# Optimization experiments

Measured on AMD Instinct MI355X. Metric: run time of the kernel, lower is better.

## Reference

```python
import jax, jax.numpy as jnp
import numpy as np

B, SQ, SK, D, H, DFF = 4, 1024, 1024, 1024, 16, 4096
DEPTH = D // H
EPS = 1e-6


def setup_inputs() -> dict:
    key = jax.random.key(0)
    ks = jax.random.split(key, 32)
    s = 0.02
    inp = {
        "x": jax.random.normal(ks[0], (B, SQ, D), jnp.float32),
        "y": jax.random.normal(ks[1], (B, SK, D), jnp.float32),
        "causality_mask": jnp.zeros((1, 1, 1, SK), jnp.float32),
        "padding_mask": jnp.zeros((1, 1, SQ, SQ), jnp.float32),
    }
    names = ["sa_wq", "sa_wk", "sa_wv", "sa_wo", "ca_wq", "ca_wk", "ca_wv", "ca_wo"]
    for i, n in enumerate(names):
        inp[n] = jax.random.normal(ks[2 + i], (D, D), jnp.float32) * s
        inp[n.replace("w", "b")] = jnp.zeros((D,), jnp.float32)
    inp["ffn_w1"] = jax.random.normal(ks[10], (D, DFF), jnp.float32) * s
    inp["ffn_b1"] = jnp.zeros((DFF,), jnp.float32)
    inp["ffn_w2"] = jax.random.normal(ks[11], (DFF, D), jnp.float32) * s
    inp["ffn_b2"] = jnp.zeros((D,), jnp.float32)
    for i, n in enumerate(["ln1", "ln2", "ln3"]):
        inp[n + "_g"] = jnp.ones((D,), jnp.float32)
        inp[n + "_b"] = jnp.zeros((D,), jnp.float32)
    return inp


def _layernorm(x, g, b):
    mu = jnp.mean(x, axis=-1, keepdims=True)
    var = jnp.mean(jnp.square(x - mu), axis=-1, keepdims=True)
    return (x - mu) * jax.lax.rsqrt(var + EPS) * g + b


def _split_heads(x):
    b, s, _ = x.shape
    return x.reshape(b, s, H, DEPTH).transpose(0, 2, 1, 3)  # [B,H,S,depth]


def _mha(q_in, k_in, v_in, mask, wq, bq, wk, bk, wv, bv, wo, bo):
    q = _split_heads(q_in @ wq + bq)
    k = _split_heads(k_in @ wk + bk)
    v = _split_heads(v_in @ wv + bv)
    scores = jnp.einsum("bhqd,bhkd->bhqk", q, k) / jnp.sqrt(jnp.float32(DEPTH))
    if mask is not None:
        scores = scores + mask * -1e9
    attn = jax.nn.softmax(scores, axis=-1)
    out = jnp.einsum("bhqk,bhkd->bhqd", attn, v)
    out = out.transpose(0, 2, 1, 3).reshape(q_in.shape[0], q_in.shape[1], D)
    return out @ wo + bo, attn


def reference(x, y, causality_mask, padding_mask,
              sa_wq, sa_bq, sa_wk, sa_bk, sa_wv, sa_bv, sa_wo, sa_bo,
              ca_wq, ca_bq, ca_wk, ca_bk, ca_wv, ca_bv, ca_wo, ca_bo,
              ffn_w1, ffn_b1, ffn_w2, ffn_b2,
              ln1_g, ln1_b, ln2_g, ln2_b, ln3_g, ln3_b):
    # self-attn sub-layer (source passes padding_mask here)
    residual = x
    out = _layernorm(x, ln1_g, ln1_b)
    out, dec_attn = _mha(out, out, out, padding_mask,
                         sa_wq, sa_bq, sa_wk, sa_bk, sa_wv, sa_bv, sa_wo, sa_bo)
    out = out + residual
    # cross-attn sub-layer (source passes causality_mask here)
    residual = out
    out2 = _layernorm(out, ln2_g, ln2_b)
    out2, dec_enc_attn = _mha(out2, y, y, causality_mask,
                              ca_wq, ca_bq, ca_wk, ca_bk, ca_wv, ca_bv, ca_wo, ca_bo)
    out = out2 + residual
    # FFN sub-layer
    residual = out
    h = _layernorm(out, ln3_g, ln3_b)
    h = jax.nn.relu(h @ ffn_w1 + ffn_b1) @ ffn_w2 + ffn_b2
    out = h + residual
    return out, dec_attn, dec_enc_attn
```

## Files before the change

### kernel.cpp

```cpp
#include <hip/hip_runtime.h>
#include <stdint.h>


typedef __attribute__((ext_vector_type(8))) short bf16x8;
typedef __attribute__((ext_vector_type(4))) float f32x4;

typedef const void __attribute__((address_space(1)))* gas_ptr;
typedef void __attribute__((address_space(3)))* las_ptr;

__device__ __forceinline__ ushort f2bf(float f) {
  union { float f; uint32_t u; } x; x.f = f;
  uint32_t r = x.u + 0x7fffu + ((x.u >> 16) & 1u);
  return (ushort)(r >> 16);
}


__global__ __launch_bounds__(256) void convert_f32_bf16(const float* __restrict__ src,
                                                        ushort* __restrict__ dst, int n4) {
  int i = blockIdx.x * 256 + threadIdx.x;
  if (i < n4) {
    float4 v = ((const float4*)src)[i];
    ushort4 o;
    o.x = f2bf(v.x); o.y = f2bf(v.y); o.z = f2bf(v.z); o.w = f2bf(v.w);
    ((ushort4*)dst)[i] = o;
  }
}

__global__ __launch_bounds__(256) void transpose_f32_bf16(const float* __restrict__ src,
                                                          ushort* __restrict__ dst,
                                                          int R, int C) {
  __shared__ ushort tile[32][33];
  int c0 = blockIdx.x * 32, r0 = blockIdx.y * 32;
  int tx = threadIdx.x, ty = threadIdx.y;
  for (int i = ty; i < 32; i += 8)
    tile[i][tx] = f2bf(src[(long)(r0 + i) * C + c0 + tx]);
  __syncthreads();
  for (int i = ty; i < 32; i += 8)
    dst[(long)(c0 + i) * R + r0 + tx] = tile[tx][i];
}

__global__ __launch_bounds__(256) void layernorm_to_bf16(const float* __restrict__ x,
                                                         const float* __restrict__ gamma,
                                                         const float* __restrict__ beta,
                                                         ushort* __restrict__ out) {
  const int row = blockIdx.x;
  const int t = threadIdx.x, lane = t & 63, w = t >> 6;
  float4 v = ((const float4*)(x + (long)row * 1024))[t];
  float s = v.x + v.y + v.z + v.w;
#pragma unroll
  for (int off = 32; off >= 1; off >>= 1) s += __shfl_xor(s, off);
  __shared__ float r1[4], r2[4];
  if (lane == 0) r1[w] = s;
  __syncthreads();
  const float mu = (r1[0] + r1[1] + r1[2] + r1[3]) * (1.f / 1024.f);
  const float dx = v.x - mu, dy = v.y - mu, dz = v.z - mu, dw = v.w - mu;
  float q = dx * dx + dy * dy + dz * dz + dw * dw;
#pragma unroll
  for (int off = 32; off >= 1; off >>= 1) q += __shfl_xor(q, off);
  if (lane == 0) r2[w] = q;
  __syncthreads();
  const float var = (r2[0] + r2[1] + r2[2] + r2[3]) * (1.f / 1024.f);
  const float is = rsqrtf(var + 1e-6f);
  float4 g4 = ((const float4*)gamma)[t];
  float4 b4 = ((const float4*)beta)[t];
  ushort4 o;
  o.x = f2bf(dx * is * g4.x + b4.x);
  o.y = f2bf(dy * is * g4.y + b4.y);
  o.z = f2bf(dz * is * g4.z + b4.z);
  o.w = f2bf(dw * is * g4.w + b4.w);
  ((ushort4*)(out + (long)row * 1024))[t] = o;
}

__global__ __launch_bounds__(256) void init_bias_res(const float* __restrict__ res,
                                                     const float* __restrict__ bias,
                                                     float* __restrict__ out, int n4) {
  int i = blockIdx.x * 256 + threadIdx.x;
  if (i < n4) {
    float4 r = ((const float4*)res)[i];
    float4 b = ((const float4*)bias)[i & 255];
    float4 o = {r.x + b.x, r.y + b.y, r.z + b.z, r.w + b.w};
    ((float4*)out)[i] = o;
  }
}


constexpr int EPI_BF16 = 0;
constexpr int EPI_F32RES = 1;
constexpr int EPI_BF16RELU = 4;
constexpr int EPI_ATOMIC = 6;

template <int BM, int BN, int EPI>
__global__ __launch_bounds__(256) void gemm_bt(const ushort* __restrict__ Aall, long sAz, int lda,
                                               const ushort* __restrict__ Ball, long sBz, int ldb,
                                               const float* __restrict__ bias,
                                               const float* __restrict__ res,
                                               void* __restrict__ outv,
                                               int M, int N, int K) {
  constexpr int BK = 32;
  constexpr int WM = BM / 2, WN = BN / 2;
  constexpr int MR = WM / 16, NR = WN / 16;
  constexpr int ACH = BM * BK / 8;
  constexpr int BCH = BN * BK / 8;

  const int z = blockIdx.z;
  const ushort* A = Aall + (long)z * sAz;
  const ushort* B = Ball + (long)z * sBz;
  const int m0 = blockIdx.x * BM;
  const int n0 = blockIdx.y * BN;

  __shared__ ushort lds[2][(BM + BN) * BK];

  const int t = threadIdx.x;
  const int lane = t & 63;
  const int w = t >> 6;
  const int wr = w >> 1, wc = w & 1;
  const int g = lane >> 4, rl = lane & 15;
  const int cbase = t & ~63;

  f32x4 acc[MR][NR];
#pragma unroll
  for (int i = 0; i < MR; ++i)
#pragma unroll
    for (int j = 0; j < NR; ++j) {
      f32x4 zv = {0.f, 0.f, 0.f, 0.f};
      acc[i][j] = zv;
    }

  auto stage = [&](int buf, int kt) {
    const int k0 = kt * BK;
#pragma unroll
    for (int j = 0; j < ACH / 256; ++j) {
      const int c = j * 256 + t;
      const int row = c >> 2, pos = c & 3;
      const int kg = pos ^ (row & 3);
      const ushort* src = A + (long)(m0 + row) * lda + k0 + kg * 8;
      ushort* dst = &lds[buf][(j * 256 + cbase) * 8];
      __builtin_amdgcn_global_load_lds((gas_ptr)src, (las_ptr)dst, 16, 0, 0);
    }
#pragma unroll
    for (int j = 0; j < BCH / 256; ++j) {
      const int c = j * 256 + t;
      const int row = c >> 2, pos = c & 3;
      const int kg = pos ^ (row & 3);
      const ushort* src = B + (long)(n0 + row) * ldb + k0 + kg * 8;
      ushort* dst = &lds[buf][BM * BK + (j * 256 + cbase) * 8];
      __builtin_amdgcn_global_load_lds((gas_ptr)src, (las_ptr)dst, 16, 0, 0);
    }
  };

  const int nt = K / BK;
  stage(0, 0);
  asm volatile("s_waitcnt vmcnt(0)" ::: "memory");
  __syncthreads();

  int cur = 0;
  for (int kt = 0; kt < nt; ++kt) {
    if (kt + 1 < nt) stage(cur ^ 1, kt + 1);
    bf16x8 af[MR], bfr[NR];
#pragma unroll
    for (int i = 0; i < MR; ++i) {
      const int row = wr * WM + i * 16 + rl;
      af[i] = *(const bf16x8*)&lds[cur][row * BK + ((g ^ (row & 3)) * 8)];
    }
#pragma unroll
    for (int j = 0; j < NR; ++j) {
      const int row = wc * WN + j * 16 + rl;
      bfr[j] = *(const bf16x8*)&lds[cur][BM * BK + row * BK + ((g ^ (row & 3)) * 8)];
    }
#pragma unroll
    for (int i = 0; i < MR; ++i)
#pragma unroll
      for (int j = 0; j < NR; ++j)
        acc[i][j] = __builtin_amdgcn_mfma_f32_16x16x32_bf16(af[i], bfr[j], acc[i][j], 0, 0, 0);
    asm volatile("s_waitcnt vmcnt(0)" ::: "memory");
    __syncthreads();
    cur ^= 1;
  }

  const bool hasb = (bias != nullptr);
#pragma unroll
  for (int i = 0; i < MR; ++i) {
#pragma unroll
    for (int j = 0; j < NR; ++j) {
#pragma unroll
      for (int e = 0; e < 4; ++e) {
        const int row = m0 + wr * WM + i * 16 + g * 4 + e;
        const int col = n0 + wc * WN + j * 16 + rl;
        float v = acc[i][j][e];
        if (hasb) v += bias[col];
        if constexpr (EPI == EPI_BF16 || EPI == EPI_BF16RELU) {
          float vv = (EPI == EPI_BF16RELU && v < 0.f) ? 0.f : v;
          ((ushort*)outv)[(long)row * N + col] = f2bf(vv);
        } else if constexpr (EPI == EPI_F32RES) {
          ((float*)outv)[(long)row * N + col] = v + res[(long)row * N + col];
        } else if constexpr (EPI == EPI_ATOMIC) {
          atomicAdd(&((float*)outv)[(long)row * N + col], v);
        }
      }
    }
  }
}


template <bool CROSS>
__global__ __launch_bounds__(256) void qkv_proj(const ushort* __restrict__ Aq,
                                                const ushort* __restrict__ Akv,
                                                const ushort* __restrict__ Wt,
                                                const float* __restrict__ bq,
                                                const float* __restrict__ bk,
                                                const float* __restrict__ bv,
                                                ushort* __restrict__ Qh,
                                                ushort* __restrict__ Kh,
                                                ushort* __restrict__ VhT) {
  constexpr int BM = 128, BN = 128, BK = 32;
  constexpr int MR = 4, NR = 4;

  const int z = blockIdx.z;
  const ushort* A = (CROSS && z > 0) ? Akv : Aq;
  const ushort* B = Wt + (long)z * 1048576;
  const float* bias = (z == 0) ? bq : (z == 1) ? bk : bv;
  const int m0 = blockIdx.x * BM;
  const int n0 = blockIdx.y * BN;

  __shared__ ushort lds[2][(BM + BN) * BK];

  const int t = threadIdx.x;
  const int lane = t & 63;
  const int w = t >> 6;
  const int wr = w >> 1, wc = w & 1;
  const int g = lane >> 4, rl = lane & 15;
  const int cbase = t & ~63;

  f32x4 acc[MR][NR];
#pragma unroll
  for (int i = 0; i < MR; ++i)
#pragma unroll
    for (int j = 0; j < NR; ++j) {
      f32x4 zv = {0.f, 0.f, 0.f, 0.f};
      acc[i][j] = zv;
    }

  auto stage = [&](int buf, int kt) {
    const int k0 = kt * BK;
    {
      const int row = t >> 2, pos = t & 3;
      const int kg = pos ^ (row & 3);
      const ushort* srcA = A + (long)(m0 + row) * 1024 + k0 + kg * 8;
      __builtin_amdgcn_global_load_lds((gas_ptr)srcA, (las_ptr)&lds[buf][cbase * 8], 16, 0, 0);
      const int c2 = 256 + t;
      const int row2 = c2 >> 2, pos2 = c2 & 3;
      const int kg2 = pos2 ^ (row2 & 3);
      const ushort* srcA2 = A + (long)(m0 + row2) * 1024 + k0 + kg2 * 8;
      __builtin_amdgcn_global_load_lds((gas_ptr)srcA2, (las_ptr)&lds[buf][(256 + cbase) * 8], 16, 0, 0);
      const ushort* srcB = B + (long)(n0 + row) * 1024 + k0 + kg * 8;
      __builtin_amdgcn_global_load_lds((gas_ptr)srcB, (las_ptr)&lds[buf][4096 + cbase * 8], 16, 0, 0);
      const ushort* srcB2 = B + (long)(n0 + row2) * 1024 + k0 + kg2 * 8;
      __builtin_amdgcn_global_load_lds((gas_ptr)srcB2, (las_ptr)&lds[buf][4096 + (256 + cbase) * 8], 16, 0, 0);
    }
  };

  stage(0, 0);
  asm volatile("s_waitcnt vmcnt(0)" ::: "memory");
  __syncthreads();

  int cur = 0;
  for (int kt = 0; kt < 32; ++kt) {
    if (kt + 1 < 32) stage(cur ^ 1, kt + 1);
    bf16x8 af[MR], bfr[NR];
#pragma unroll
    for (int i = 0; i < MR; ++i) {
      const int row = wr * 64 + i * 16 + rl;
      af[i] = *(const bf16x8*)&lds[cur][row * BK + ((g ^ (row & 3)) * 8)];
    }
#pragma unroll
    for (int j = 0; j < NR; ++j) {
      const int row = wc * 64 + j * 16 + rl;
      bfr[j] = *(const bf16x8*)&lds[cur][4096 + row * BK + ((g ^ (row & 3)) * 8)];
    }
#pragma unroll
    for (int i = 0; i < MR; ++i)
#pragma unroll
      for (int j = 0; j < NR; ++j)
        acc[i][j] = __builtin_amdgcn_mfma_f32_16x16x32_bf16(af[i], bfr[j], acc[i][j], 0, 0, 0);
    asm volatile("s_waitcnt vmcnt(0)" ::: "memory");
    __syncthreads();
    cur ^= 1;
  }

  ushort* out = (z == 0) ? Qh : (z == 1) ? Kh : VhT;
#pragma unroll
  for (int i = 0; i < MR; ++i) {
#pragma unroll
    for (int j = 0; j < NR; ++j) {
#pragma unroll
      for (int e = 0; e < 4; ++e) {
        const int row = m0 + wr * 64 + i * 16 + g * 4 + e;
        const int col = n0 + wc * 64 + j * 16 + rl;
        const float v = acc[i][j][e] + bias[col];
        const int b = row >> 10, s = row & 1023, h = col >> 6, d = col & 63;
        if (z < 2)
          out[(((long)(b * 16 + h) * 1024) + s) * 64 + d] = f2bf(v);
        else
          out[((long)(b * 16 + h) * 64 + d) * 1024 + s] = f2bf(v);
      }
    }
  }
}


__device__ __forceinline__ int p_off(int r, int p) {
  return (r * 128 + (p ^ (r & 7))) * 8;
}

template <int MODE>
__global__ __launch_bounds__(512) void attn_softmax_pv(const ushort* __restrict__ Q,
                                                       const ushort* __restrict__ Kh,
                                                       const ushort* __restrict__ VhT,
                                                       const float* __restrict__ mask,
                                                       float* __restrict__ outF,
                                                       ushort* __restrict__ ctx) {
  const int bh = blockIdx.y;
  const int q0 = blockIdx.x * 32;
  const int t = threadIdx.x, lane = t & 63, w = t >> 6;
  const int g = lane >> 4, rl = lane & 15;
  const ushort* Qb = Q + (long)bh * 65536;
  const ushort* Kb = Kh + (long)bh * 65536;
  const ushort* Vb = VhT + (long)bh * 65536;

  __shared__ ushort Pl[32768];
  __shared__ float redm[8][32];
  __shared__ float reds[8][32];

  bf16x8 qa[2][2];
#pragma unroll
  for (int rb = 0; rb < 2; ++rb)
#pragma unroll
    for (int kk = 0; kk < 2; ++kk)
      qa[rb][kk] = *(const bf16x8*)(Qb + (long)(q0 + rb * 16 + rl) * 64 + kk * 32 + g * 8);

  f32x4 acc[2][8];
#pragma unroll
  for (int rb = 0; rb < 2; ++rb)
#pragma unroll
    for (int nf = 0; nf < 8; ++nf) {
      f32x4 zv = {0.f, 0.f, 0.f, 0.f};
      acc[rb][nf] = zv;
    }

  const int c0 = w * 128;
#pragma unroll
  for (int nf = 0; nf < 8; ++nf) {
    const ushort* kp = Kb + (long)(c0 + nf * 16 + rl) * 64 + g * 8;
    bf16x8 k0 = *(const bf16x8*)(kp);
    bf16x8 k1 = *(const bf16x8*)(kp + 32);
#pragma unroll
    for (int rb = 0; rb < 2; ++rb) {
      acc[rb][nf] = __builtin_amdgcn_mfma_f32_16x16x32_bf16(qa[rb][0], k0, acc[rb][nf], 0, 0, 0);
      acc[rb][nf] = __builtin_amdgcn_mfma_f32_16x16x32_bf16(qa[rb][1], k1, acc[rb][nf], 0, 0, 0);
    }
  }

#pragma unroll
  for (int rb = 0; rb < 2; ++rb)
#pragma unroll
    for (int nf = 0; nf < 8; ++nf)
#pragma unroll
      for (int e = 0; e < 4; ++e) {
        const int r = q0 + rb * 16 + g * 4 + e;
        const int c = c0 + nf * 16 + rl;
        float mv;
        if constexpr (MODE == 0) mv = mask[(long)r * 1024 + c];
        else mv = mask[c];
        acc[rb][nf][e] = acc[rb][nf][e] * 0.125f + mv * (-1e9f);
      }

  float mrow[2][4];
#pragma unroll
  for (int rb = 0; rb < 2; ++rb)
#pragma unroll
    for (int e = 0; e < 4; ++e) {
      float m = acc[rb][0][e];
#pragma unroll
      for (int nf = 1; nf < 8; ++nf) m = fmaxf(m, acc[rb][nf][e]);
#pragma unroll
      for (int off = 8; off >= 1; off >>= 1) m = fmaxf(m, __shfl_xor(m, off));
      mrow[rb][e] = m;
    }
  if (rl == 0)
#pragma unroll
    for (int rb = 0; rb < 2; ++rb)
#pragma unroll
      for (int e = 0; e < 4; ++e) redm[w][rb * 16 + g * 4 + e] = mrow[rb][e];
  __syncthreads();
  float mfin[2][4];
#pragma unroll
  for (int rb = 0; rb < 2; ++rb)
#pragma unroll
    for (int e = 0; e < 4; ++e) {
      const int r = rb * 16 + g * 4 + e;
      float m = redm[0][r];
#pragma unroll
      for (int ww = 1; ww < 8; ++ww) m = fmaxf(m, redm[ww][r]);
      mfin[rb][e] = m;
    }

  float srow[2][4];
#pragma unroll
  for (int rb = 0; rb < 2; ++rb)
#pragma unroll
    for (int e = 0; e < 4; ++e) {
      float s = 0.f;
#pragma unroll
      for (int nf = 0; nf < 8; ++nf) {
        float p = exp2f((acc[rb][nf][e] - mfin[rb][e]) * 1.44269504088896340736f);
        acc[rb][nf][e] = p;
        s += p;
      }
#pragma unroll
      for (int off = 8; off >= 1; off >>= 1) s += __shfl_xor(s, off);
      srow[rb][e] = s;
    }
  if (rl == 0)
#pragma unroll
    for (int rb = 0; rb < 2; ++rb)
#pragma unroll
      for (int e = 0; e < 4; ++e) reds[w][rb * 16 + g * 4 + e] = srow[rb][e];
  __syncthreads();

#pragma unroll
  for (int rb = 0; rb < 2; ++rb)
#pragma unroll
    for (int e = 0; e < 4; ++e) {
      const int r = rb * 16 + g * 4 + e;
      float s = 0.f;
#pragma unroll
      for (int ww = 0; ww < 8; ++ww) s += reds[ww][r];
      const float inv = 1.0f / s;
      const long rowoff = (long)bh * 1048576 + (long)(q0 + r) * 1024;
#pragma unroll
      for (int nf = 0; nf < 8; ++nf) {
        const int c = c0 + nf * 16 + rl;
        const float p = acc[rb][nf][e] * inv;
        outF[rowoff + c] = p;
        Pl[p_off(r, c >> 3) + (c & 7)] = f2bf(p);
      }
    }
  __syncthreads();

  f32x4 acc2[2][4];
#pragma unroll
  for (int rb = 0; rb < 2; ++rb)
#pragma unroll
    for (int j = 0; j < 4; ++j) {
      f32x4 zv = {0.f, 0.f, 0.f, 0.f};
      acc2[rb][j] = zv;
    }
#pragma unroll
  for (int s = 0; s < 4; ++s) {
    const int kb = c0 + s * 32;
    bf16x8 a[2];
#pragma unroll
    for (int rb = 0; rb < 2; ++rb)
      a[rb] = *(const bf16x8*)&Pl[p_off(rb * 16 + rl, (kb >> 3) + g)];
#pragma unroll
    for (int j = 0; j < 4; ++j) {
      bf16x8 b = *(const bf16x8*)(Vb + (long)(j * 16 + rl) * 1024 + kb + g * 8);
#pragma unroll
      for (int rb = 0; rb < 2; ++rb)
        acc2[rb][j] = __builtin_amdgcn_mfma_f32_16x16x32_bf16(a[rb], b, acc2[rb][j], 0, 0, 0);
    }
  }
  __syncthreads();

  float* Pred = (float*)Pl;
#pragma unroll
  for (int rb = 0; rb < 2; ++rb)
#pragma unroll
    for (int j = 0; j < 4; ++j)
#pragma unroll
      for (int e = 0; e < 4; ++e) {
        const int r = rb * 16 + g * 4 + e;
        const int d = j * 16 + rl;
        Pred[w * 2048 + r * 64 + d] = acc2[rb][j][e];
      }
  __syncthreads();

  const int bb = bh >> 4, hh = bh & 15;
#pragma unroll
  for (int i = t; i < 2048; i += 512) {
    float s = 0.f;
#pragma unroll
    for (int ww = 0; ww < 8; ++ww) s += Pred[ww * 2048 + i];
    const int r = i >> 6, d = i & 63;
    ctx[((long)bb * 1024 + q0 + r) * 1024 + hh * 64 + d] = f2bf(s);
  }
}


extern "C" void kernel_launch(void* const* d_in, const int* in_sizes, int n_in,
                              void* d_out, int out_size, void* d_ws, size_t ws_size,
                              hipStream_t stream) {
  (void)in_sizes; (void)n_in; (void)out_size; (void)ws_size;

  const float* x     = (const float*)d_in[0];
  const float* y     = (const float*)d_in[1];
  const float* cmask = (const float*)d_in[2];
  const float* pmask = (const float*)d_in[3];
  const float* sa_wq = (const float*)d_in[4];
  const float* sa_bq = (const float*)d_in[5];
  const float* sa_wk = (const float*)d_in[6];
  const float* sa_bk = (const float*)d_in[7];
  const float* sa_wv = (const float*)d_in[8];
  const float* sa_bv = (const float*)d_in[9];
  const float* sa_wo = (const float*)d_in[10];
  const float* sa_bo = (const float*)d_in[11];
  const float* ca_wq = (const float*)d_in[12];
  const float* ca_bq = (const float*)d_in[13];
  const float* ca_wk = (const float*)d_in[14];
  const float* ca_bk = (const float*)d_in[15];
  const float* ca_wv = (const float*)d_in[16];
  const float* ca_bv = (const float*)d_in[17];
  const float* ca_wo = (const float*)d_in[18];
  const float* ca_bo = (const float*)d_in[19];
  const float* ffn_w1 = (const float*)d_in[20];
  const float* ffn_b1 = (const float*)d_in[21];
  const float* ffn_w2 = (const float*)d_in[22];
  const float* ffn_b2 = (const float*)d_in[23];
  const float* ln1_g = (const float*)d_in[24];
  const float* ln1_b = (const float*)d_in[25];
  const float* ln2_g = (const float*)d_in[26];
  const float* ln2_b = (const float*)d_in[27];
  const float* ln3_g = (const float*)d_in[28];
  const float* ln3_b = (const float*)d_in[29];

  char* ws = (char*)d_ws;
  ushort* wT0 = (ushort*)(ws + 0);
  ushort* w1T = (ushort*)(ws + (16L << 20));
  ushort* w2T = (ushort*)(ws + (24L << 20));
  ushort* ybf = (ushort*)(ws + (32L << 20));
  ushort* lnb = (ushort*)(ws + (40L << 20));
  ushort* Qh  = (ushort*)(ws + (48L << 20));
  ushort* Kh  = (ushort*)(ws + (56L << 20));
  ushort* VhT = (ushort*)(ws + (64L << 20));
  ushort* ctx = (ushort*)(ws + (72L << 20));
  float*  out1 = (float*)(ws + (80L << 20));
  float*  out2 = (float*)(ws + (96L << 20));
  ushort* hbuf = (ushort*)(ws + (112L << 20));

  float* out0   = (float*)d_out;
  float* attnF1 = out0 + 4194304;
  float* attnF2 = out0 + 71303168;

  convert_f32_bf16<<<dim3(4096), dim3(256), 0, stream>>>(y, ybf, 1048576);
  const float* wsrc[8] = {sa_wq, sa_wk, sa_wv, sa_wo, ca_wq, ca_wk, ca_wv, ca_wo};
  for (int i = 0; i < 8; ++i)
    transpose_f32_bf16<<<dim3(32, 32), dim3(32, 8), 0, stream>>>(wsrc[i], wT0 + (long)i * 1048576, 1024, 1024);
  transpose_f32_bf16<<<dim3(128, 32), dim3(32, 8), 0, stream>>>(ffn_w1, w1T, 1024, 4096);
  transpose_f32_bf16<<<dim3(32, 128), dim3(32, 8), 0, stream>>>(ffn_w2, w2T, 4096, 1024);

  layernorm_to_bf16<<<dim3(4096), dim3(256), 0, stream>>>(x, ln1_g, ln1_b, lnb);

  qkv_proj<false><<<dim3(32, 8, 3), dim3(256), 0, stream>>>(
      lnb, lnb, wT0, sa_bq, sa_bk, sa_bv, Qh, Kh, VhT);

  attn_softmax_pv<0><<<dim3(32, 64), dim3(512), 0, stream>>>(Qh, Kh, VhT, pmask, attnF1, ctx);

  init_bias_res<<<dim3(4096), dim3(256), 0, stream>>>(x, sa_bo, out1, 1048576);
  gemm_bt<128, 128, EPI_ATOMIC><<<dim3(32, 8, 2), dim3(256), 0, stream>>>(
      ctx, 512L, 1024, wT0 + 3L * 1048576, 512L, 1024, nullptr, nullptr, out1, 4096, 1024, 512);

  layernorm_to_bf16<<<dim3(4096), dim3(256), 0, stream>>>(out1, ln2_g, ln2_b, lnb);

  qkv_proj<true><<<dim3(32, 8, 3), dim3(256), 0, stream>>>(
      lnb, ybf, wT0 + 4L * 1048576, ca_bq, ca_bk, ca_bv, Qh, Kh, VhT);

  attn_softmax_pv<1><<<dim3(32, 64), dim3(512), 0, stream>>>(Qh, Kh, VhT, cmask, attnF2, ctx);

  init_bias_res<<<dim3(4096), dim3(256), 0, stream>>>(out1, ca_bo, out2, 1048576);
  gemm_bt<128, 128, EPI_ATOMIC><<<dim3(32, 8, 2), dim3(256), 0, stream>>>(
      ctx, 512L, 1024, wT0 + 7L * 1048576, 512L, 1024, nullptr, nullptr, out2, 4096, 1024, 512);

  layernorm_to_bf16<<<dim3(4096), dim3(256), 0, stream>>>(out2, ln3_g, ln3_b, lnb);

  gemm_bt<128, 128, EPI_BF16RELU><<<dim3(32, 32, 1), dim3(256), 0, stream>>>(
      lnb, 0L, 1024, w1T, 0L, 1024, ffn_b1, nullptr, hbuf, 4096, 4096, 1024);

  init_bias_res<<<dim3(4096), dim3(256), 0, stream>>>(out2, ffn_b2, out0, 1048576);
  gemm_bt<128, 128, EPI_ATOMIC><<<dim3(32, 8, 4), dim3(256), 0, stream>>>(
      hbuf, 1024L, 4096, w2T, 1024L, 4096, nullptr, nullptr, out0, 4096, 1024, 1024);
}
```

Baseline: 1.212 ms.

## Deepen GEMM pipeline, replace atomics with partial-sum reduce+LN, add XCD tile mapping

The GEMM and QKV projection kernels now use a 4-buffer LDS ring with three stages in flight and vmcnt-based waits, instead of double buffering with a full drain every step. Split-K output GEMMs write per-split partials instead of doing float atomics. A new fused reduce_ln kernel sums the partials, adds bias and residual, and applies the next LayerNorm, which removes the init_bias_res and separate layernorm launches. Blocks are remapped so neighbouring tiles land on the same XCD for L2 reuse, the 8 weight transposes are batched into one launch, and the V-transpose epilogue stores packed ushort4. The partial buffers cost extra memory traffic and workspace, and the hard-coded vmcnt constants depend on the static_assert that each stage issues 4 loads.

```diff
diff --git a/kernel.cpp b/kernel.cpp
--- a/kernel.cpp
+++ b/kernel.cpp
@@ -24,6 +24,21 @@
     o.x = f2bf(v.x); o.y = f2bf(v.y); o.z = f2bf(v.z); o.w = f2bf(v.w);
     ((ushort4*)dst)[i] = o;
   }
+}
+
+struct Ptr8 { const float* p[8]; };
+
+__global__ __launch_bounds__(256) void transpose8_f32_bf16(Ptr8 srcs, ushort* __restrict__ dst) {
+  __shared__ ushort tile[32][33];
+  const float* src = srcs.p[blockIdx.z];
+  ushort* d = dst + (long)blockIdx.z * 1048576;
+  int c0 = blockIdx.x * 32, r0 = blockIdx.y * 32;
+  int tx = threadIdx.x, ty = threadIdx.y;
+  for (int i = ty; i < 32; i += 8)
+    tile[i][tx] = f2bf(src[(long)(r0 + i) * 1024 + c0 + tx]);
+  __syncthreads();
+  for (int i = ty; i < 32; i += 8)
+    d[(long)(c0 + i) * 1024 + r0 + tx] = tile[tx][i];
 }
 
 __global__ __launch_bounds__(256) void transpose_f32_bf16(const float* __restrict__ src,
@@ -71,29 +86,71 @@
   ((ushort4*)(out + (long)row * 1024))[t] = o;
 }
 
-__global__ __launch_bounds__(256) void init_bias_res(const float* __restrict__ res,
-                                                     const float* __restrict__ bias,
-                                                     float* __restrict__ out, int n4) {
-  int i = blockIdx.x * 256 + threadIdx.x;
-  if (i < n4) {
-    float4 r = ((const float4*)res)[i];
-    float4 b = ((const float4*)bias)[i & 255];
-    float4 o = {r.x + b.x, r.y + b.y, r.z + b.z, r.w + b.w};
-    ((float4*)out)[i] = o;
-  }
-}
-
-
-constexpr int EPI_BF16 = 0;
-constexpr int EPI_F32RES = 1;
-constexpr int EPI_BF16RELU = 4;
-constexpr int EPI_ATOMIC = 6;
-
-template <int BM, int BN, int EPI>
+template <int NP, bool DO_LN>
+__global__ __launch_bounds__(256) void reduce_ln(const float* __restrict__ part,
+                                                 const float* __restrict__ res,
+                                                 const float* __restrict__ bias,
+                                                 const float* __restrict__ g,
+                                                 const float* __restrict__ b,
+                                                 float* __restrict__ outres,
+                                                 ushort* __restrict__ outln) {
+  const int row = blockIdx.x;
+  const int t = threadIdx.x, lane = t & 63, w = t >> 6;
+  const long base = (long)row * 256 + t;
+  float4 v = ((const float4*)res)[base];
+  float4 bi = ((const float4*)bias)[t];
+  v.x += bi.x; v.y += bi.y; v.z += bi.z; v.w += bi.w;
+#pragma unroll
+  for (int p = 0; p < NP; ++p) {
+    float4 pv = ((const float4*)part)[(long)p * 1048576 + base];
+    v.x += pv.x; v.y += pv.y; v.z += pv.z; v.w += pv.w;
+  }
+  ((float4*)outres)[base] = v;
+  if constexpr (DO_LN) {
+    float s = v.x + v.y + v.z + v.w;
+#pragma unroll
+    for (int off = 32; off >= 1; off >>= 1) s += __shfl_xor(s, off);
+    __shared__ float r1[4], r2[4];
+    if (lane == 0) r1[w] = s;
+    __syncthreads();
+    const float mu = (r1[0] + r1[1] + r1[2] + r1[3]) * (1.f / 1024.f);
+    const float dx = v.x - mu, dy = v.y - mu, dz = v.z - mu, dw = v.w - mu;
+    float q = dx * dx + dy * dy + dz * dz + dw * dw;
+#pragma unroll
+    for (int off = 32; off >= 1; off >>= 1) q += __shfl_xor(q, off);
+    if (lane == 0) r2[w] = q;
+    __syncthreads();
+    const float var = (r2[0] + r2[1] + r2[2] + r2[3]) * (1.f / 1024.f);
+    const float is = rsqrtf(var + 1e-6f);
+    float4 g4 = ((const float4*)g)[t];
+    float4 b4 = ((const float4*)b)[t];
+    ushort4 o;
+    o.x = f2bf(dx * is * g4.x + b4.x);
+    o.y = f2bf(dy * is * g4.y + b4.y);
+    o.z = f2bf(dz * is * g4.z + b4.z);
+    o.w = f2bf(dw * is * g4.w + b4.w);
+    ((ushort4*)outln)[base] = o;
+  }
+}
+
+template <int MS, int NS>
+__device__ __forceinline__ void xcd_map(int& mi, int& ni) {
+  const int GX = gridDim.x;
+  const int bid = blockIdx.x + GX * blockIdx.y;
+  const int xcd = bid & 7, idx = bid >> 3;
+  const int mw = GX / MS;
+  mi = (xcd % MS) * mw + idx % mw;
+  ni = (xcd / MS) * (gridDim.y / NS) + idx / mw;
+}
+
+
+constexpr int EPI_BF16RELU = 0;
+constexpr int EPI_PARTIAL = 1;
+
+template <int BM, int BN, int EPI, int MS, int NS>
 __global__ __launch_bounds__(256) void gemm_bt(const ushort* __restrict__ Aall, long sAz, int lda,
                                                const ushort* __restrict__ Ball, long sBz, int ldb,
                                                const float* __restrict__ bias,
-                                               const float* __restrict__ res,
                                                void* __restrict__ outv,
                                                int M, int N, int K) {
   constexpr int BK = 32;
@@ -101,14 +158,18 @@
   constexpr int MR = WM / 16, NR = WN / 16;
   constexpr int ACH = BM * BK / 8;
   constexpr int BCH = BN * BK / 8;
+  constexpr int BUFSZ = (BM + BN) * BK;
+  static_assert((ACH + BCH) / 256 == 4, "LPT must be 4 for vmcnt constants");
 
   const int z = blockIdx.z;
   const ushort* A = Aall + (long)z * sAz;
   const ushort* B = Ball + (long)z * sBz;
-  const int m0 = blockIdx.x * BM;
-  const int n0 = blockIdx.y * BN;
-
-  __shared__ ushort lds[2][(BM + BN) * BK];
+  int mi, ni;
+  xcd_map<MS, NS>(mi, ni);
+  const int m0 = mi * BM;
+  const int n0 = ni * BN;
+
+  __shared__ ushort lds[4 * BUFSZ];
 
   const int t = threadIdx.x;
   const int lane = t & 63;
@@ -128,56 +189,60 @@
 
   auto stage = [&](int buf, int kt) {
     const int k0 = kt * BK;
-#pragma unroll
-    for (int j = 0; j < ACH / 256; ++j) {
+    ushort* lb = &lds[buf * BUFSZ];
+#pragma unroll
+    for (int j = 0; j < 2; ++j) {
       const int c = j * 256 + t;
       const int row = c >> 2, pos = c & 3;
       const int kg = pos ^ (row & 3);
       const ushort* src = A + (long)(m0 + row) * lda + k0 + kg * 8;
-      ushort* dst = &lds[buf][(j * 256 + cbase) * 8];
-      __builtin_amdgcn_global_load_lds((gas_ptr)src, (las_ptr)dst, 16, 0, 0);
-    }
-#pragma unroll
-    for (int j = 0; j < BCH / 256; ++j) {
+      __builtin_amdgcn_global_load_lds((gas_ptr)src, (las_ptr)&lb[(j * 256 + cbase) * 8], 16, 0, 0);
+    }
+#pragma unroll
+    for (int j = 0; j < 2; ++j) {
       const int c = j * 256 + t;
       const int row = c >> 2, pos = c & 3;
       const int kg = pos ^ (row & 3);
       const ushort* src = B + (long)(n0 + row) * ldb + k0 + kg * 8;
-      ushort* dst = &lds[buf][BM * BK + (j * 256 + cbase) * 8];
-      __builtin_amdgcn_global_load_lds((gas_ptr)src, (las_ptr)dst, 16, 0, 0);
+      __builtin_amdgcn_global_load_lds((gas_ptr)src, (las_ptr)&lb[BM * BK + (j * 256 + cbase) * 8], 16, 0, 0);
     }
   };
 
   const int nt = K / BK;
   stage(0, 0);
-  asm volatile("s_waitcnt vmcnt(0)" ::: "memory");
-  __syncthreads();
-
-  int cur = 0;
+  if (nt > 1) stage(1, 1);
+  if (nt > 2) stage(2, 2);
+
   for (int kt = 0; kt < nt; ++kt) {
-    if (kt + 1 < nt) stage(cur ^ 1, kt + 1);
+    const int rem = nt - 1 - kt;
+    if (rem >= 2)      asm volatile("s_waitcnt vmcnt(8)" ::: "memory");
+    else if (rem == 1) asm volatile("s_waitcnt vmcnt(4)" ::: "memory");
+    else               asm volatile("s_waitcnt vmcnt(0)" ::: "memory");
+    __builtin_amdgcn_s_barrier();
+    asm volatile("" ::: "memory");
+    const ushort* buf = &lds[(kt & 3) * BUFSZ];
     bf16x8 af[MR], bfr[NR];
 #pragma unroll
     for (int i = 0; i < MR; ++i) {
       const int row = wr * WM + i * 16 + rl;
-      af[i] = *(const bf16x8*)&lds[cur][row * BK + ((g ^ (row & 3)) * 8)];
+      af[i] = *(const bf16x8*)&buf[row * BK + ((g ^ (row & 3)) * 8)];
     }
 #pragma unroll
     for (int j = 0; j < NR; ++j) {
       const int row = wc * WN + j * 16 + rl;
-      bfr[j] = *(const bf16x8*)&lds[cur][BM * BK + row * BK + ((g ^ (row & 3)) * 8)];
+      bfr[j] = *(const bf16x8*)&buf[BM * BK + row * BK + ((g ^ (row & 3)) * 8)];
     }
 #pragma unroll
     for (int i = 0; i < MR; ++i)
 #pragma unroll
       for (int j = 0; j < NR; ++j)
         acc[i][j] = __builtin_amdgcn_mfma_f32_16x16x32_bf16(af[i], bfr[j], acc[i][j], 0, 0, 0);
-    asm volatile("s_waitcnt vmcnt(0)" ::: "memory");
-    __syncthreads();
-    cur ^= 1;
-  }
-
-  const bool hasb = (bias != nullptr);
+    asm volatile("s_waitcnt lgkmcnt(0)" ::: "memory");
+    __builtin_amdgcn_s_barrier();
+    asm volatile("" ::: "memory");
+    if (kt + 3 < nt) stage((kt + 3) & 3, kt + 3);
+  }
+
 #pragma unroll
   for (int i = 0; i < MR; ++i) {
 #pragma unroll
@@ -187,14 +252,11 @@
         const int row = m0 + wr * WM + i * 16 + g * 4 + e;
         const int col = n0 + wc * WN + j * 16 + rl;
         float v = acc[i][j][e];
-        if (hasb) v += bias[col];
-        if constexpr (EPI == EPI_BF16 || EPI == EPI_BF16RELU) {
-          float vv = (EPI == EPI_BF16RELU && v < 0.f) ? 0.f : v;
-          ((ushort*)outv)[(long)row * N + col] = f2bf(vv);
-        } else if constexpr (EPI == EPI_F32RES) {
-          ((float*)outv)[(long)row * N + col] = v + res[(long)row * N + col];
-        } else if constexpr (EPI == EPI_ATOMIC) {
-          atomicAdd(&((float*)outv)[(long)row * N + col], v);
+        if constexpr (EPI == EPI_BF16RELU) {
+          v += bias[col];
+          ((ushort*)outv)[(long)row * N + col] = f2bf(v < 0.f ? 0.f : v);
+        } else {
+          ((float*)outv)[(long)z * M * N + (long)row * N + col] = v;
         }
       }
     }
@@ -214,15 +276,18 @@
                                                 ushort* __restrict__ VhT) {
   constexpr int BM = 128, BN = 128, BK = 32;
   constexpr int MR = 4, NR = 4;
+  constexpr int BUFSZ = (BM + BN) * BK;
 
   const int z = blockIdx.z;
   const ushort* A = (CROSS && z > 0) ? Akv : Aq;
   const ushort* B = Wt + (long)z * 1048576;
   const float* bias = (z == 0) ? bq : (z == 1) ? bk : bv;
-  const int m0 = blockIdx.x * BM;
-  const int n0 = blockIdx.y * BN;
-
-  __shared__ ushort lds[2][(BM + BN) * BK];
+  int mi, ni;
+  xcd_map<4, 2>(mi, ni);
+  const int m0 = mi * BM;
+  const int n0 = ni * BN;
+
+  __shared__ ushort lds[4 * BUFSZ];
 
   const int t = threadIdx.x;
   const int lane = t & 63;
@@ -242,49 +307,57 @@
 
   auto stage = [&](int buf, int kt) {
     const int k0 = kt * BK;
-    {
-      const int row = t >> 2, pos = t & 3;
+    ushort* lb = &lds[buf * BUFSZ];
+#pragma unroll
+    for (int j = 0; j < 2; ++j) {
+      const int c = j * 256 + t;
+      const int row = c >> 2, pos = c & 3;
       const int kg = pos ^ (row & 3);
-      const ushort* srcA = A + (long)(m0 + row) * 1024 + k0 + kg * 8;
-      __builtin_amdgcn_global_load_lds((gas_ptr)srcA, (las_ptr)&lds[buf][cbase * 8], 16, 0, 0);
-      const int c2 = 256 + t;
-      const int row2 = c2 >> 2, pos2 = c2 & 3;
-      const int kg2 = pos2 ^ (row2 & 3);
-      const ushort* srcA2 = A + (long)(m0 + row2) * 1024 + k0 + kg2 * 8;
-      __builtin_amdgcn_global_load_lds((gas_ptr)srcA2, (las_ptr)&lds[buf][(256 + cbase) * 8], 16, 0, 0);
-      const ushort* srcB = B + (long)(n0 + row) * 1024 + k0 + kg * 8;
-      __builtin_amdgcn_global_load_lds((gas_ptr)srcB, (las_ptr)&lds[buf][4096 + cbase * 8], 16, 0, 0);
-      const ushort* srcB2 = B + (long)(n0 + row2) * 1024 + k0 + kg2 * 8;
-      __builtin_amdgcn_global_load_lds((gas_ptr)srcB2, (las_ptr)&lds[buf][4096 + (256 + cbase) * 8], 16, 0, 0);
+      const ushort* src = A + (long)(m0 + row) * 1024 + k0 + kg * 8;
+      __builtin_amdgcn_global_load_lds((gas_ptr)src, (las_ptr)&lb[(j * 256 + cbase) * 8], 16, 0, 0);
+    }
+#pragma unroll
+    for (int j = 0; j < 2; ++j) {
+      const int c = j * 256 + t;
+      const int row = c >> 2, pos = c & 3;
+      const int kg = pos ^ (row & 3);
+      const ushort* src = B + (long)(n0 + row) * 1024 + k0 + kg * 8;
+      __builtin_amdgcn_global_load_lds((gas_ptr)src, (las_ptr)&lb[BM * BK + (j * 256 + cbase) * 8], 16, 0, 0);
     }
   };
 
   stage(0, 0);
-  asm volatile("s_waitcnt vmcnt(0)" ::: "memory");
-  __syncthreads();
-
-  int cur = 0;
+  stage(1, 1);
+  stage(2, 2);
+
   for (int kt = 0; kt < 32; ++kt) {
-    if (kt + 1 < 32) stage(cur ^ 1, kt + 1);
+    const int rem = 31 - kt;
+    if (rem >= 2)      asm volatile("s_waitcnt vmcnt(8)" ::: "memory");
+    else if (rem == 1) asm volatile("s_waitcnt vmcnt(4)" ::: "memory");
+    else               asm volatile("s_waitcnt vmcnt(0)" ::: "memory");
+    __builtin_amdgcn_s_barrier();
+    asm volatile("" ::: "memory");
+    const ushort* buf = &lds[(kt & 3) * BUFSZ];
     bf16x8 af[MR], bfr[NR];
 #pragma unroll
     for (int i = 0; i < MR; ++i) {
       const int row = wr * 64 + i * 16 + rl;
-      af[i] = *(const bf16x8*)&lds[cur][row * BK + ((g ^ (row & 3)) * 8)];
+      af[i] = *(const bf16x8*)&buf[row * BK + ((g ^ (row & 3)) * 8)];
     }
 #pragma unroll
     for (int j = 0; j < NR; ++j) {
       const int row = wc * 64 + j * 16 + rl;
-      bfr[j] = *(const bf16x8*)&lds[cur][4096 + row * BK + ((g ^ (row & 3)) * 8)];
+      bfr[j] = *(const bf16x8*)&buf[BM * BK + row * BK + ((g ^ (row & 3)) * 8)];
     }
 #pragma unroll
     for (int i = 0; i < MR; ++i)
 #pragma unroll
       for (int j = 0; j < NR; ++j)
         acc[i][j] = __builtin_amdgcn_mfma_f32_16x16x32_bf16(af[i], bfr[j], acc[i][j], 0, 0, 0);
-    asm volatile("s_waitcnt vmcnt(0)" ::: "memory");
-    __syncthreads();
-    cur ^= 1;
+    asm volatile("s_waitcnt lgkmcnt(0)" ::: "memory");
+    __builtin_amdgcn_s_barrier();
+    asm volatile("" ::: "memory");
+    if (kt + 3 < 32) stage((kt + 3) & 3, kt + 3);
   }
 
   ushort* out = (z == 0) ? Qh : (z == 1) ? Kh : VhT;
@@ -292,16 +365,22 @@
   for (int i = 0; i < MR; ++i) {
 #pragma unroll
     for (int j = 0; j < NR; ++j) {
-#pragma unroll
-      for (int e = 0; e < 4; ++e) {
-        const int row = m0 + wr * 64 + i * 16 + g * 4 + e;
-        const int col = n0 + wc * 64 + j * 16 + rl;
-        const float v = acc[i][j][e] + bias[col];
-        const int b = row >> 10, s = row & 1023, h = col >> 6, d = col & 63;
-        if (z < 2)
-          out[(((long)(b * 16 + h) * 1024) + s) * 64 + d] = f2bf(v);
-        else
-          out[((long)(b * 16 + h) * 64 + d) * 1024 + s] = f2bf(v);
+      const int row0 = m0 + wr * 64 + i * 16 + g * 4;
+      const int col = n0 + wc * 64 + j * 16 + rl;
+      const int b = row0 >> 10, h = col >> 6, d = col & 63;
+      if (z == 2) {
+        ushort4 pk;
+        pk.x = f2bf(acc[i][j][0] + bias[col]);
+        pk.y = f2bf(acc[i][j][1] + bias[col]);
+        pk.z = f2bf(acc[i][j][2] + bias[col]);
+        pk.w = f2bf(acc[i][j][3] + bias[col]);
+        *(ushort4*)&out[((long)(b * 16 + h) * 64 + d) * 1024 + (row0 & 1023)] = pk;
+      } else {
+#pragma unroll
+        for (int e = 0; e < 4; ++e) {
+          const int s = (row0 + e) & 1023;
+          out[(((long)(b * 16 + h) * 1024) + s) * 64 + d] = f2bf(acc[i][j][e] + bias[col]);
+        }
       }
     }
   }
@@ -319,8 +398,11 @@
                                                        const float* __restrict__ mask,
                                                        float* __restrict__ outF,
                                                        ushort* __restrict__ ctx) {
-  const int bh = blockIdx.y;
-  const int q0 = blockIdx.x * 32;
+  const int bid = blockIdx.x + 32 * blockIdx.y;
+  const int xcd = bid & 7, idx = bid >> 3;
+  const int q0 = (idx & 31) * 32;
+  const int bh = xcd * 8 + (idx >> 5);
+
   const int t = threadIdx.x, lane = t & 63, w = t >> 6;
   const int g = lane >> 4, rl = lane & 15;
   const ushort* Qb = Q + (long)bh * 65536;
@@ -546,15 +628,15 @@
   float*  out1 = (float*)(ws + (80L << 20));
   float*  out2 = (float*)(ws + (96L << 20));
   ushort* hbuf = (ushort*)(ws + (112L << 20));
+  float*  part = (float*)(ws + (152L << 20));
 
   float* out0   = (float*)d_out;
   float* attnF1 = out0 + 4194304;
   float* attnF2 = out0 + 71303168;
 
   convert_f32_bf16<<<dim3(4096), dim3(256), 0, stream>>>(y, ybf, 1048576);
-  const float* wsrc[8] = {sa_wq, sa_wk, sa_wv, sa_wo, ca_wq, ca_wk, ca_wv, ca_wo};
-  for (int i = 0; i < 8; ++i)
-    transpose_f32_bf16<<<dim3(32, 32), dim3(32, 8), 0, stream>>>(wsrc[i], wT0 + (long)i * 1048576, 1024, 1024);
+  Ptr8 w8 = {{sa_wq, sa_wk, sa_wv, sa_wo, ca_wq, ca_wk, ca_wv, ca_wo}};
+  transpose8_f32_bf16<<<dim3(32, 32, 8), dim3(32, 8), 0, stream>>>(w8, wT0);
   transpose_f32_bf16<<<dim3(128, 32), dim3(32, 8), 0, stream>>>(ffn_w1, w1T, 1024, 4096);
   transpose_f32_bf16<<<dim3(32, 128), dim3(32, 8), 0, stream>>>(ffn_w2, w2T, 4096, 1024);
 
@@ -565,27 +647,26 @@
 
   attn_softmax_pv<0><<<dim3(32, 64), dim3(512), 0, stream>>>(Qh, Kh, VhT, pmask, attnF1, ctx);
 
-  init_bias_res<<<dim3(4096), dim3(256), 0, stream>>>(x, sa_bo, out1, 1048576);
-  gemm_bt<128, 128, EPI_ATOMIC><<<dim3(32, 8, 2), dim3(256), 0, stream>>>(
-      ctx, 512L, 1024, wT0 + 3L * 1048576, 512L, 1024, nullptr, nullptr, out1, 4096, 1024, 512);
-
-  layernorm_to_bf16<<<dim3(4096), dim3(256), 0, stream>>>(out1, ln2_g, ln2_b, lnb);
+  gemm_bt<128, 128, EPI_PARTIAL, 4, 2><<<dim3(32, 8, 2), dim3(256), 0, stream>>>(
+      ctx, 512L, 1024, wT0 + 3L * 1048576, 512L, 1024, nullptr, part, 4096, 1024, 512);
+  reduce_ln<2, true><<<dim3(4096), dim3(256), 0, stream>>>(
+      part, x, sa_bo, ln2_g, ln2_b, out1, lnb);
 
   qkv_proj<true><<<dim3(32, 8, 3), dim3(256), 0, stream>>>(
       lnb, ybf, wT0 + 4L * 1048576, ca_bq, ca_bk, ca_bv, Qh, Kh, VhT);
 
   attn_softmax_pv<1><<<dim3(32, 64), dim3(512), 0, stream>>>(Qh, Kh, VhT, cmask, attnF2, ctx);
 
-  init_bias_res<<<dim3(4096), dim3(256), 0, stream>>>(out1, ca_bo, out2, 1048576);
-  gemm_bt<128, 128, EPI_ATOMIC><<<dim3(32, 8, 2), dim3(256), 0, stream>>>(
-      ctx, 512L, 1024, wT0 + 7L * 1048576, 512L, 1024, nullptr, nullptr, out2, 4096, 1024, 512);
-
-  layernorm_to_bf16<<<dim3(4096), dim3(256), 0, stream>>>(out2, ln3_g, ln3_b, lnb);
-
-  gemm_bt<128, 128, EPI_BF16RELU><<<dim3(32, 32, 1), dim3(256), 0, stream>>>(
-      lnb, 0L, 1024, w1T, 0L, 1024, ffn_b1, nullptr, hbuf, 4096, 4096, 1024);
-
-  init_bias_res<<<dim3(4096), dim3(256), 0, stream>>>(out2, ffn_b2, out0, 1048576);
-  gemm_bt<128, 128, EPI_ATOMIC><<<dim3(32, 8, 4), dim3(256), 0, stream>>>(
-      hbuf, 1024L, 4096, w2T, 1024L, 4096, nullptr, nullptr, out0, 4096, 1024, 1024);
-}
+  gemm_bt<128, 128, EPI_PARTIAL, 4, 2><<<dim3(32, 8, 2), dim3(256), 0, stream>>>(
+      ctx, 512L, 1024, wT0 + 7L * 1048576, 512L, 1024, nullptr, part, 4096, 1024, 512);
+  reduce_ln<2, true><<<dim3(4096), dim3(256), 0, stream>>>(
+      part, out1, ca_bo, ln3_g, ln3_b, out2, lnb);
+
+  gemm_bt<128, 128, EPI_BF16RELU, 2, 4><<<dim3(32, 32, 1), dim3(256), 0, stream>>>(
+      lnb, 0L, 1024, w1T, 0L, 1024, ffn_b1, hbuf, 4096, 4096, 1024);
+
+  gemm_bt<128, 128, EPI_PARTIAL, 4, 2><<<dim3(32, 8, 4), dim3(256), 0, stream>>>(
+      hbuf, 1024L, 4096, w2T, 1024L, 4096, nullptr, part, 4096, 1024, 1024);
+  reduce_ln<4, false><<<dim3(4096), dim3(256), 0, stream>>>(
+      part, out2, ffn_b2, nullptr, nullptr, out0, nullptr);
+}
```

Result: faster. 1.085 ms (-10.5%).
